# Kernel optimization log

Hardware: AMD Instinct MI355X
Metric: run time of the kernel (lower is better)

The kernel has to match this reference:

```python
import jax, jax.numpy as jnp
import numpy as np

N_SPECIAL = 4
LABEL_ID = 3
C_ACT = 64
C_TIME = 32
ACT_START = N_SPECIAL
TIME_START = N_SPECIAL + C_ACT
VOCAB = TIME_START + C_TIME  # 100
B, T, D = 8, 2048, 256


def l2norm(x, eps=1e-12):
    n = jnp.sqrt(jnp.sum(x * x, axis=-1, keepdims=True))
    return x / jnp.maximum(n, eps)


def causal_proto(h_norm, is_label, nxt, lo, hi, E_cls, alpha):
    """At every <LABEL> position L, build per-class prototypes from earlier
    support label positions (class = next token at that position), add a
    Bayesian prior alpha*E_cls, and return cosine sims of h_norm[L] vs protos.
    Non-label positions (or labels with no earlier support) -> zeros.
    Implemented as a single causal scan over time (online running sums)."""
    Bv, Tv, Dv = h_norm.shape
    C = E_cls.shape[0]
    is_sup = is_label & (nxt >= lo) & (nxt < hi)          # [B,T]
    cls = jnp.clip(nxt - lo, 0, C - 1)                    # [B,T]

    def step(carry, xs):
        Hsum, cnt = carry                                  # [B,C,D], [B,C]
        h_t, cls_t, sup_t, lab_t = xs                      # [B,D],[B],[B],[B]
        proto = l2norm((Hsum + alpha * E_cls) / (cnt[:, :, None] + alpha + 1e-8))
        sims = jnp.einsum('bd,bcd->bc', h_t, proto)        # cosine (h_t is unit)
        valid = lab_t & (jnp.sum(cnt, axis=-1) > 0)        # any earlier support
        out = jnp.where(valid[:, None], sims, 0.0)
        oh = jax.nn.one_hot(cls_t, C, dtype=h_t.dtype) * sup_t[:, None].astype(h_t.dtype)
        Hsum = Hsum + oh[:, :, None] * h_t[:, None, :]
        cnt = cnt + oh
        return (Hsum, cnt), out

    init = (jnp.zeros((Bv, C, Dv), h_norm.dtype), jnp.zeros((Bv, C), h_norm.dtype))
    xs = (jnp.swapaxes(h_norm, 0, 1), jnp.swapaxes(cls, 0, 1),
          jnp.swapaxes(is_sup, 0, 1), jnp.swapaxes(is_label, 0, 1))
    _, outs = jax.lax.scan(jax.checkpoint(step), init, xs)
    return jnp.swapaxes(outs, 0, 1)                        # [B,T,C]


def setup_inputs() -> dict:
    key = jax.random.key(0)
    ks = jax.random.split(key, 6)
    f32 = jnp.float32
    return {
        'tokens': jax.random.randint(ks[0], (B, T), 0, VOCAB, dtype=jnp.int32),
        'h': jax.random.normal(ks[1], (B, T, D), dtype=f32),
        'E': jax.random.normal(ks[2], (VOCAB, D), dtype=f32) * 0.02,
        'W_next': jax.random.normal(ks[3], (C_ACT, D), dtype=f32) * 0.02,
        'b_next': jnp.zeros((C_ACT,), f32),
        'W_time': jax.random.normal(ks[4], (C_TIME, D), dtype=f32) * 0.02,
        'b_time': jnp.zeros((C_TIME,), f32),
        'tied_scale_act': jnp.array(0.0, f32),
        'tied_scale_time': jnp.array(0.0, f32),
        'proto_scale_act': jnp.array(1.0, f32),
        'proto_scale_time': jnp.array(1.0, f32),
        'proto_prior_act': jnp.array(0.5, f32),
        'proto_prior_time': jnp.array(0.5, f32),
        'proto_temp_act': jnp.array(1.0, f32),
        'proto_temp_time': jnp.array(1.0, f32),
    }


def reference(tokens, h, E, W_next, b_next, W_time, b_time,
              tied_scale_act, tied_scale_time, proto_scale_act, proto_scale_time,
              proto_prior_act, proto_prior_time, proto_temp_act, proto_temp_time):
    sp = jax.nn.softplus
    # parametric heads
    param_next = jnp.einsum('btd,cd->btc', h, W_next) + b_next
    param_time = jnp.einsum('btd,cd->btc', h, W_time) + b_time
    # weight-tied heads (gradient flows into E here)
    tied_act = jnp.einsum('btd,cd->btc', h, E[ACT_START:TIME_START])
    tied_time = jnp.einsum('btd,cd->btc', h, E[TIME_START:VOCAB])
    # prototype head (E detached, as in the torch code)
    h_norm = l2norm(h)
    E_det = jax.lax.stop_gradient(E)
    E_act = l2norm(E_det[ACT_START:TIME_START])
    E_time = l2norm(E_det[TIME_START:VOCAB])
    nxt = jnp.roll(tokens, -1, axis=1)
    is_label = tokens == LABEL_ID
    proto_act = causal_proto(h_norm, is_label, nxt, ACT_START, TIME_START,
                             E_act, sp(proto_prior_act)) * sp(proto_temp_act)
    proto_time = causal_proto(h_norm, is_label, nxt, TIME_START, VOCAB,
                              E_time, sp(proto_prior_time)) * sp(proto_temp_time)
    activity_logits = param_next + sp(tied_scale_act) * tied_act + sp(proto_scale_act) * proto_act
    time_logits = param_time + sp(tied_scale_time) * tied_time + sp(proto_scale_time) * proto_time
    return (activity_logits, time_logits)
```

## Files before the change

kernel.cpp:

```cpp
#include <hip/hip_runtime.h>
#include <hip/hip_bf16.h>

#define Bv 8
#define Tv 2048
#define Dv 256
#define C_ACT 64
#define C_TIME 32
#define NCLS 96
#define LABEL_ID 3
#define ACT_START 4
#define TIME_START 68
#define VOCAB 100
#define MAXEV 36

typedef short bf16x8 __attribute__((ext_vector_type(8)));
typedef float f32x4  __attribute__((ext_vector_type(4)));

__device__ __forceinline__ float bf2f(__hip_bfloat16 x) { return __bfloat162float(x); }
__device__ __forceinline__ float bfb(unsigned short u) {
    union { unsigned int i; float f; } x; x.i = ((unsigned int)u) << 16; return x.f;
}
__device__ __forceinline__ short f2bs(float x) {
    __hip_bfloat16 b = __float2bfloat16(x);
    return *reinterpret_cast<short*>(&b);
}
__device__ __forceinline__ float spf(float x) { return log1pf(expf(x)); }

__device__ __forceinline__ float ldx(const void* p, size_t i, bool f32) {
    return f32 ? ((const float*)p)[i] : bf2f(((const __hip_bfloat16*)p)[i]);
}
__device__ __forceinline__ void stx(void* p, size_t i, float v, bool f32) {
    if (f32) ((float*)p)[i] = v;
    else     ((__hip_bfloat16*)p)[i] = __float2bfloat16(v);
}
__device__ __forceinline__ float4 ld4(const void* p, size_t i, bool f32) {
    if (f32) return *reinterpret_cast<const float4*>((const float*)p + i);
    ushort4 s = *reinterpret_cast<const ushort4*>((const unsigned short*)p + i);
    float4 u; u.x = bfb(s.x); u.y = bfb(s.y); u.z = bfb(s.z); u.w = bfb(s.w);
    return u;
}

__device__ __forceinline__ bool detect_f32_256(const void* h, int tid, int* s_cnt)
{
    if (tid == 0) *s_cnt = 0;
    __syncthreads();
    ushort4 u = *(reinterpret_cast<const ushort4*>(h) + tid);
    int c = 0; float v;
    v = bfb(u.x); if (!(fabsf(v) < 1e20f)) c++;
    v = bfb(u.y); if (!(fabsf(v) < 1e20f)) c++;
    v = bfb(u.z); if (!(fabsf(v) < 1e20f)) c++;
    v = bfb(u.w); if (!(fabsf(v) < 1e20f)) c++;
    #pragma unroll
    for (int o = 32; o > 0; o >>= 1) c += __shfl_down(c, o);
    if ((tid & 63) == 0 && c) atomicAdd(s_cnt, c);
    __syncthreads();
    return *s_cnt >= 4;
}

__device__ __forceinline__ size_t out_idx(int b, int L, int c)
{
    return (c < C_ACT)
        ? ((size_t)(b * Tv + L) * C_ACT + c)
        : ((size_t)Bv * Tv * C_ACT + (size_t)(b * Tv + L) * C_TIME + (c - C_ACT));
}

#define K1_ROWS 32
#define HPAD 72
#define EVLD 264
#define GLD 44

__global__ __launch_bounds__(256) void k_all(
    const int* __restrict__ tokens,
    const void* __restrict__ h,
    const void* __restrict__ E,
    const void* __restrict__ Wn, const void* __restrict__ bn,
    const void* __restrict__ Wt, const void* __restrict__ bt,
    const void* ts_a, const void* ts_t,
    const void* ps_a, const void* ps_t,
    const void* pp_a, const void* pp_t,
    const void* pt_a, const void* pt_t,
    void* __restrict__ out)
{
    __shared__ union {
        struct { short hB[K1_ROWS * HPAD]; short mB[NCLS * HPAD]; } t;
        struct {
            unsigned short hb[48][EVLD];
            union {
                unsigned short AsMs[48][EVLD];
                struct {
                    float Gl[MAXEV][GLD];
                    float P[MAXEV][24];
                    float Pm[MAXEV][24];
                    float SG[MAXEV][24];
                } r;
            } u2;
            float nrm[MAXEV];
        } s;
    } u;
    __shared__ int s_pos[MAXEV], s_cls[MAXEV];
    __shared__ int s_cnt, s_evn;

    int tid = threadIdx.x;
    bool f32 = detect_f32_256(h, tid, &s_cnt);
    float spt_a = spf(ldx(ts_a, 0, f32));
    float spt_t = spf(ldx(ts_t, 0, f32));

    if (blockIdx.x >= 32) {
        int R0   = (blockIdx.x - 32) * K1_ROWS;
        int w    = tid >> 6;
        int lane = tid & 63;
        int lr   = lane & 15;
        int quad = lane >> 4;
        int rt   = w & 1;
        int cg   = w >> 1;

        f32x4 acc[3];
        #pragma unroll
        for (int n = 0; n < 3; ++n) acc[n] = (f32x4){0.f, 0.f, 0.f, 0.f};

        for (int dc = 0; dc < 4; ++dc) {
            #pragma unroll
            for (int k = 0; k < 2; ++k) {
                int f = tid + k * 256;
                int row = f >> 4, dd4 = f & 15;
                float4 v = ld4(h, (size_t)(R0 + row) * Dv + dc * 64 + dd4 * 4, f32);
                short4 s4 = make_short4(f2bs(v.x), f2bs(v.y), f2bs(v.z), f2bs(v.w));
                *reinterpret_cast<short4*>(&u.t.hB[row * HPAD + dd4 * 4]) = s4;
            }
            #pragma unroll
            for (int k = 0; k < 6; ++k) {
                int f = tid + k * 256;
                int c = f >> 4, dd4 = f & 15;
                int col = dc * 64 + dd4 * 4;
                bool act = c < C_ACT;
                size_t wrow = act ? (size_t)c : (size_t)(c - C_ACT);
                int erow = act ? (ACT_START + c) : (TIME_START + (c - C_ACT));
                float4 w4 = ld4(act ? Wn : Wt, wrow * Dv + col, f32);
                float4 e4 = ld4(E, (size_t)erow * Dv + col, f32);
                float spt = act ? spt_a : spt_t;
                short4 s4 = make_short4(f2bs(w4.x + spt * e4.x),
                                        f2bs(w4.y + spt * e4.y),
                                        f2bs(w4.z + spt * e4.z),
                                        f2bs(w4.w + spt * e4.w));
                *reinterpret_cast<short4*>(&u.t.mB[c * HPAD + dd4 * 4]) = s4;
            }
            __syncthreads();

            #pragma unroll
            for (int ks = 0; ks < 2; ++ks) {
                int k0 = ks * 32;
                bf16x8 a = *reinterpret_cast<const bf16x8*>(
                    &u.t.hB[(16 * rt + lr) * HPAD + k0 + quad * 8]);
                #pragma unroll
                for (int nn = 0; nn < 3; ++nn) {
                    int n = 3 * cg + nn;
                    bf16x8 bf = *reinterpret_cast<const bf16x8*>(
                        &u.t.mB[(16 * n + lr) * HPAD + k0 + quad * 8]);
                    acc[nn] = __builtin_amdgcn_mfma_f32_16x16x32_bf16(a, bf, acc[nn], 0, 0, 0);
                }
            }
            __syncthreads();
        }

        #pragma unroll
        for (int nn = 0; nn < 3; ++nn) {
            int c = 16 * (3 * cg + nn) + lr;
            float bias = (c < C_ACT) ? ldx(bn, c, f32) : ldx(bt, c - C_ACT, f32);
            #pragma unroll
            for (int r = 0; r < 4; ++r) {
                int row = R0 + 16 * rt + quad * 4 + r;
                if (tokens[row] == LABEL_ID) continue;
                stx(out, out_idx(row >> 11, row & (Tv - 1), c), acc[nn][r] + bias, f32);
            }
        }
        return;
    }

    int b  = blockIdx.x >> 2;
    int q  = blockIdx.x & 3;
    int c0 = q * 24;
    int lane = tid & 63, wvx = tid >> 6;
    int lr = lane & 15, quad = lane >> 4;

    int* s_tok = reinterpret_cast<int*>(&u.s.u2.AsMs[0][0]);
    for (int i = tid; i < Tv; i += 256) s_tok[i] = tokens[(size_t)b * Tv + i];
    __syncthreads();

    if (tid < 64) {
        int base = 0;
        for (int seg = 0; seg < 32; ++seg) {
            unsigned long long m = __ballot(s_tok[seg * 64 + tid] == LABEL_ID);
            int rank = __popcll(m & ((1ull << tid) - 1ull));
            if (((m >> tid) & 1ull) && (base + rank) < MAXEV)
                s_pos[base + rank] = seg * 64 + tid;
            base += __popcll(m);
        }
        if (tid == 0) s_evn = base < MAXEV ? base : MAXEV;
    }
    __syncthreads();
    int evn = s_evn;
    int nrt = (evn + 15) >> 4;

    if (tid < evn) {
        int nxt = s_tok[(s_pos[tid] + 1) & (Tv - 1)];
        int c = -1;
        if (nxt >= ACT_START && nxt < TIME_START)  c = nxt - ACT_START;
        else if (nxt >= TIME_START && nxt < VOCAB) c = C_ACT + (nxt - TIME_START);
        s_cls[tid] = c;
    }

    {
        float4 hv[9];
        #pragma unroll
        for (int k = 0; k < 9; ++k) {
            int i = wvx + 4 * k;
            if (i < evn)
                hv[k] = ld4(h, ((size_t)b * Tv + s_pos[i]) * Dv + lane * 4, f32);
        }
        #pragma unroll
        for (int k = 0; k < 9; ++k) {
            int i = wvx + 4 * k;
            if (i < evn) {
                float4 v = hv[k];
                float p = v.x * v.x + v.y * v.y + v.z * v.z + v.w * v.w;
                #pragma unroll
                for (int o = 32; o > 0; o >>= 1) p += __shfl_xor(p, o);
                float nr = fmaxf(sqrtf(p), 1e-12f);
                float inv = 1.0f / nr;
                ushort4 s4;
                s4.x = (unsigned short)f2bs(v.x * inv);
                s4.y = (unsigned short)f2bs(v.y * inv);
                s4.z = (unsigned short)f2bs(v.z * inv);
                s4.w = (unsigned short)f2bs(v.w * inv);
                *reinterpret_cast<ushort4*>(&u.s.hb[i][lane * 4]) = s4;
                if (lane == 0) u.s.nrm[i] = nr;
            }
        }
        for (int i = evn + wvx; i < 16 * nrt; i += 4) {
            ushort4 z; z.x = z.y = z.z = z.w = 0;
            *reinterpret_cast<ushort4*>(&u.s.hb[i][lane * 4]) = z;
        }
    }
    __syncthreads();

    float alpha_a = spf(ldx(pp_a, 0, f32));
    float alpha_t = spf(ldx(pp_t, 0, f32));

    {
        float4 ev[6], wv6[6];
        #pragma unroll
        for (int k = 0; k < 6; ++k) {
            int lc = wvx + 4 * k, c = c0 + lc;
            bool act = c < C_ACT;
            int erow = act ? (ACT_START + c) : (TIME_START + (c - C_ACT));
            size_t wrow = act ? (size_t)c : (size_t)(c - C_ACT);
            ev[k]  = ld4(E, (size_t)erow * Dv + lane * 4, f32);
            wv6[k] = ld4(act ? Wn : Wt, wrow * Dv + lane * 4, f32);
        }
        #pragma unroll
        for (int k = 0; k < 6; ++k) {
            int lc = wvx + 4 * k, c = c0 + lc;
            bool act = c < C_ACT;
            float4 e4 = ev[k], w4 = wv6[k];
            float p = e4.x * e4.x + e4.y * e4.y + e4.z * e4.z + e4.w * e4.w;
            #pragma unroll
            for (int o = 32; o > 0; o >>= 1) p += __shfl_xor(p, o);
            float alpha = act ? alpha_a : alpha_t;
            float ai  = alpha / fmaxf(sqrtf(p), 1e-12f);
            float spt = act ? spt_a : spt_t;
            ushort4 a4, m4;
            a4.x = (unsigned short)f2bs(e4.x * ai);
            a4.y = (unsigned short)f2bs(e4.y * ai);
            a4.z = (unsigned short)f2bs(e4.z * ai);
            a4.w = (unsigned short)f2bs(e4.w * ai);
            m4.x = (unsigned short)f2bs(w4.x + spt * e4.x);
            m4.y = (unsigned short)f2bs(w4.y + spt * e4.y);
            m4.z = (unsigned short)f2bs(w4.z + spt * e4.z);
            m4.w = (unsigned short)f2bs(w4.w + spt * e4.w);
            *reinterpret_cast<ushort4*>(&u.s.u2.AsMs[lc][lane * 4])      = a4;
            *reinterpret_cast<ushort4*>(&u.s.u2.AsMs[24 + lc][lane * 4]) = m4;
        }
    }
    __syncthreads();

    {
        int nct = 3 + nrt;
        int TT  = nrt * nct;
        f32x4 accs[5];
        #pragma unroll
        for (int kk = 0; kk < 5; ++kk) {
            int t = wvx + 4 * kk;
            if (t < TT) {
                int rt2 = t / nct, ct = t - rt2 * nct;
                int ar = 16 * rt2 + lr;
                const unsigned short* bbase = (ct < 3)
                    ? &u.s.u2.AsMs[16 * ct + lr][0]
                    : &u.s.hb[16 * (ct - 3) + lr][0];
                f32x4 acc = (f32x4){0.f, 0.f, 0.f, 0.f};
                #pragma unroll
                for (int ks = 0; ks < 8; ++ks) {
                    bf16x8 a  = *reinterpret_cast<const bf16x8*>(
                        &u.s.hb[ar][ks * 32 + quad * 8]);
                    bf16x8 bf = *reinterpret_cast<const bf16x8*>(
                        &bbase[ks * 32 + quad * 8]);
                    acc = __builtin_amdgcn_mfma_f32_16x16x32_bf16(a, bf, acc, 0, 0, 0);
                }
                accs[kk] = acc;
            }
        }
        __syncthreads();
        #pragma unroll
        for (int kk = 0; kk < 5; ++kk) {
            int t = wvx + 4 * kk;
            if (t < TT) {
                int rt2 = t / nct, ct = t - rt2 * nct;
                #pragma unroll
                for (int r = 0; r < 4; ++r) {
                    int row = 16 * rt2 + quad * 4 + r;
                    if (row >= evn) continue;
                    if (ct < 3) {
                        int cc = 16 * ct + lr;
                        if (cc < 24) u.s.u2.r.P[row][cc] = accs[kk][r];
                        else         u.s.u2.r.Pm[row][cc - 24] = accs[kk][r];
                    } else {
                        int j = 16 * (ct - 3) + lr;
                        if (j < evn) u.s.u2.r.Gl[row][j] = accs[kk][r];
                    }
                }
            }
        }
    }
    __syncthreads();

    for (int t = tid; t < evn * 24; t += 256) {
        int i = t / 24, lc = t - i * 24;
        int c = c0 + lc;
        float s = 0.f;
        for (int j = 0; j < i; ++j)
            s += (s_cls[j] == c) ? u.s.u2.r.Gl[i][j] : 0.f;
        u.s.u2.r.SG[i][lc] = s;
    }
    __syncthreads();

    {
        float mult_a = spf(ldx(ps_a, 0, f32)) * spf(ldx(pt_a, 0, f32));
        float mult_t = spf(ldx(ps_t, 0, f32)) * spf(ldx(pt_t, 0, f32));
        for (int t = tid; t < evn * 24; t += 256) {
            int i = t / 24, lc = t - i * 24;
            int c = c0 + lc;
            bool actc = c < C_ACT;
            float alpha = actc ? alpha_a : alpha_t;
            float bias  = actc ? ldx(bn, c, f32) : ldx(bt, c - C_ACT, f32);
            float mult  = actc ? mult_a : mult_t;
            float n2 = alpha * alpha;
            bool any = false;
            for (int j = 0; j < i; ++j) {
                int cj = s_cls[j];
                if (cj == c)
                    n2 += 2.f * (u.s.u2.r.P[j][lc] + u.s.u2.r.SG[j][lc])
                        + u.s.u2.r.Gl[j][j];
                any = any || (actc ? (cj >= 0 && cj < C_ACT) : (cj >= C_ACT));
            }
            float v = u.s.u2.r.Pm[i][lc] * u.s.nrm[i] + bias;
            if (any) {
                float num = u.s.u2.r.P[i][lc] + u.s.u2.r.SG[i][lc];
                v += mult * (num / fmaxf(sqrtf(n2), 1e-20f));
            }
            stx(out, out_idx(b, s_pos[i], c), v, f32);
        }
    }
}

extern "C" void kernel_launch(void* const* d_in, const int* in_sizes, int n_in,
                              void* d_out, int out_size, void* d_ws, size_t ws_size,
                              hipStream_t stream)
{
    const int* tokens = (const int*)d_in[0];
    const void* h    = d_in[1];
    const void* E    = d_in[2];
    const void* Wn   = d_in[3];
    const void* bn   = d_in[4];
    const void* Wt   = d_in[5];
    const void* bt   = d_in[6];
    const void* ts_a = d_in[7];
    const void* ts_t = d_in[8];
    const void* ps_a = d_in[9];
    const void* ps_t = d_in[10];
    const void* pp_a = d_in[11];
    const void* pp_t = d_in[12];
    const void* pt_a = d_in[13];
    const void* pt_t = d_in[14];

    k_all<<<32 + (Bv * Tv) / K1_ROWS, 256, 0, stream>>>(
        tokens, h, E, Wn, bn, Wt, bt,
        ts_a, ts_t, ps_a, ps_t, pp_a, pp_t, pt_a, pt_t, d_out);
}
```

Baseline: 117.9 us.

## Double-buffer LDS tiles and prefetch bf16 inputs in parametric GEMM blocks

For bf16 inputs, the dense-head GEMM blocks now use two LDS buffers. Global loads for the next K-chunk are issued into registers with 16-byte vector loads before the MFMAs on the current chunk, which removes one barrier per iteration and overlaps load latency with compute. Token and bias loads are hoisted ahead of the main loop. The fp32 path keeps the old single-buffer scheme, and the doubled LDS footprint for this branch shares the union with the proto branch's larger buffers.

```diff
diff --git a/kernel.cpp b/kernel.cpp
--- a/kernel.cpp
+++ b/kernel.cpp
@@ -15,6 +15,7 @@
 
 typedef short bf16x8 __attribute__((ext_vector_type(8)));
 typedef float f32x4  __attribute__((ext_vector_type(4)));
+typedef unsigned short u16x8 __attribute__((ext_vector_type(8)));
 
 __device__ __forceinline__ float bf2f(__hip_bfloat16 x) { return __bfloat162float(x); }
 __device__ __forceinline__ float bfb(unsigned short u) {
@@ -82,7 +83,10 @@
     void* __restrict__ out)
 {
     __shared__ union {
-        struct { short hB[K1_ROWS * HPAD]; short mB[NCLS * HPAD]; } t;
+        struct {
+            short hB[2][K1_ROWS * HPAD];
+            short mB[2][NCLS * HPAD];
+        } t;
         struct {
             unsigned short hb[48][EVLD];
             union {
@@ -118,59 +122,141 @@
         #pragma unroll
         for (int n = 0; n < 3; ++n) acc[n] = (f32x4){0.f, 0.f, 0.f, 0.f};
 
-        for (int dc = 0; dc < 4; ++dc) {
-            #pragma unroll
-            for (int k = 0; k < 2; ++k) {
-                int f = tid + k * 256;
-                int row = f >> 4, dd4 = f & 15;
-                float4 v = ld4(h, (size_t)(R0 + row) * Dv + dc * 64 + dd4 * 4, f32);
-                short4 s4 = make_short4(f2bs(v.x), f2bs(v.y), f2bs(v.z), f2bs(v.w));
-                *reinterpret_cast<short4*>(&u.t.hB[row * HPAD + dd4 * 4]) = s4;
-            }
-            #pragma unroll
-            for (int k = 0; k < 6; ++k) {
-                int f = tid + k * 256;
-                int c = f >> 4, dd4 = f & 15;
-                int col = dc * 64 + dd4 * 4;
-                bool act = c < C_ACT;
-                size_t wrow = act ? (size_t)c : (size_t)(c - C_ACT);
-                int erow = act ? (ACT_START + c) : (TIME_START + (c - C_ACT));
-                float4 w4 = ld4(act ? Wn : Wt, wrow * Dv + col, f32);
-                float4 e4 = ld4(E, (size_t)erow * Dv + col, f32);
-                float spt = act ? spt_a : spt_t;
-                short4 s4 = make_short4(f2bs(w4.x + spt * e4.x),
-                                        f2bs(w4.y + spt * e4.y),
-                                        f2bs(w4.z + spt * e4.z),
-                                        f2bs(w4.w + spt * e4.w));
-                *reinterpret_cast<short4*>(&u.t.mB[c * HPAD + dd4 * 4]) = s4;
-            }
-            __syncthreads();
-
-            #pragma unroll
-            for (int ks = 0; ks < 2; ++ks) {
-                int k0 = ks * 32;
-                bf16x8 a = *reinterpret_cast<const bf16x8*>(
-                    &u.t.hB[(16 * rt + lr) * HPAD + k0 + quad * 8]);
-                #pragma unroll
-                for (int nn = 0; nn < 3; ++nn) {
-                    int n = 3 * cg + nn;
-                    bf16x8 bf = *reinterpret_cast<const bf16x8*>(
-                        &u.t.mB[(16 * n + lr) * HPAD + k0 + quad * 8]);
-                    acc[nn] = __builtin_amdgcn_mfma_f32_16x16x32_bf16(a, bf, acc[nn], 0, 0, 0);
-                }
-            }
-            __syncthreads();
-        }
-
+        int rowb = 16 * rt + quad * 4;
+        int tk[4]; float bs[3];
+        #pragma unroll
+        for (int r = 0; r < 4; ++r) tk[r] = tokens[R0 + rowb + r];
         #pragma unroll
         for (int nn = 0; nn < 3; ++nn) {
             int c = 16 * (3 * cg + nn) + lr;
-            float bias = (c < C_ACT) ? ldx(bn, c, f32) : ldx(bt, c - C_ACT, f32);
+            bs[nn] = (c < C_ACT) ? ldx(bn, c, f32) : ldx(bt, c - C_ACT, f32);
+        }
+
+        if (!f32) {
+            const unsigned short* hp  = (const unsigned short*)h;
+            const unsigned short* wnp = (const unsigned short*)Wn;
+            const unsigned short* wtp = (const unsigned short*)Wt;
+            const unsigned short* ep  = (const unsigned short*)E;
+
+            int rowh = tid >> 3, c8h = (tid & 7) * 8;
+            int hoff = (R0 + rowh) * Dv + c8h;
+
+            int cM[3], c8M[3], woff[3], eoff[3]; float sptM[3];
+            const unsigned short* wp[3];
+            #pragma unroll
+            for (int k = 0; k < 3; ++k) {
+                int f = tid + k * 256;
+                int c = f >> 3, c8 = (f & 7) * 8;
+                bool act = c < C_ACT;
+                cM[k] = c; c8M[k] = c8;
+                wp[k]   = act ? wnp : wtp;
+                woff[k] = (act ? c : c - C_ACT) * Dv + c8;
+                eoff[k] = (act ? (ACT_START + c) : (TIME_START + (c - C_ACT))) * Dv + c8;
+                sptM[k] = act ? spt_a : spt_t;
+            }
+
+            u16x8 hr, wr0, wr1, wr2, er0, er1, er2;
+            auto ldall = [&](int dc) {
+                int o = dc * 64;
+                hr  = *reinterpret_cast<const u16x8*>(hp + hoff + o);
+                wr0 = *reinterpret_cast<const u16x8*>(wp[0] + woff[0] + o);
+                er0 = *reinterpret_cast<const u16x8*>(ep + eoff[0] + o);
+                wr1 = *reinterpret_cast<const u16x8*>(wp[1] + woff[1] + o);
+                er1 = *reinterpret_cast<const u16x8*>(ep + eoff[1] + o);
+                wr2 = *reinterpret_cast<const u16x8*>(wp[2] + woff[2] + o);
+                er2 = *reinterpret_cast<const u16x8*>(ep + eoff[2] + o);
+            };
+            auto wrall = [&](int bsel) {
+                *reinterpret_cast<u16x8*>(&u.t.hB[bsel][rowh * HPAD + c8h]) = hr;
+                u16x8 m8;
+                #pragma unroll
+                for (int j = 0; j < 8; ++j)
+                    m8[j] = (unsigned short)f2bs(bfb(wr0[j]) + sptM[0] * bfb(er0[j]));
+                *reinterpret_cast<u16x8*>(&u.t.mB[bsel][cM[0] * HPAD + c8M[0]]) = m8;
+                #pragma unroll
+                for (int j = 0; j < 8; ++j)
+                    m8[j] = (unsigned short)f2bs(bfb(wr1[j]) + sptM[1] * bfb(er1[j]));
+                *reinterpret_cast<u16x8*>(&u.t.mB[bsel][cM[1] * HPAD + c8M[1]]) = m8;
+                #pragma unroll
+                for (int j = 0; j < 8; ++j)
+                    m8[j] = (unsigned short)f2bs(bfb(wr2[j]) + sptM[2] * bfb(er2[j]));
+                *reinterpret_cast<u16x8*>(&u.t.mB[bsel][cM[2] * HPAD + c8M[2]]) = m8;
+            };
+
+            ldall(0); wrall(0);
+            __syncthreads();
+            for (int dc = 0; dc < 4; ++dc) {
+                if (dc < 3) ldall(dc + 1);
+                const short* hbuf = u.t.hB[dc & 1];
+                const short* mbuf = u.t.mB[dc & 1];
+                #pragma unroll
+                for (int ks = 0; ks < 2; ++ks) {
+                    int k0 = ks * 32;
+                    bf16x8 a = *reinterpret_cast<const bf16x8*>(
+                        &hbuf[(16 * rt + lr) * HPAD + k0 + quad * 8]);
+                    #pragma unroll
+                    for (int nn = 0; nn < 3; ++nn) {
+                        bf16x8 bfv = *reinterpret_cast<const bf16x8*>(
+                            &mbuf[(16 * (3 * cg + nn) + lr) * HPAD + k0 + quad * 8]);
+                        acc[nn] = __builtin_amdgcn_mfma_f32_16x16x32_bf16(a, bfv, acc[nn], 0, 0, 0);
+                    }
+                }
+                if (dc < 3) wrall((dc + 1) & 1);
+                __syncthreads();
+            }
+        } else {
+            for (int dc = 0; dc < 4; ++dc) {
+                #pragma unroll
+                for (int k = 0; k < 2; ++k) {
+                    int f = tid + k * 256;
+                    int row = f >> 4, dd4 = f & 15;
+                    float4 v = ld4(h, (size_t)(R0 + row) * Dv + dc * 64 + dd4 * 4, f32);
+                    short4 s4 = make_short4(f2bs(v.x), f2bs(v.y), f2bs(v.z), f2bs(v.w));
+                    *reinterpret_cast<short4*>(&u.t.hB[0][row * HPAD + dd4 * 4]) = s4;
+                }
+                #pragma unroll
+                for (int k = 0; k < 6; ++k) {
+                    int f = tid + k * 256;
+                    int c = f >> 4, dd4 = f & 15;
+                    int col = dc * 64 + dd4 * 4;
+                    bool act = c < C_ACT;
+                    size_t wrow = act ? (size_t)c : (size_t)(c - C_ACT);
+                    int erow = act ? (ACT_START + c) : (TIME_START + (c - C_ACT));
+                    float4 w4 = ld4(act ? Wn : Wt, wrow * Dv + col, f32);
+                    float4 e4 = ld4(E, (size_t)erow * Dv + col, f32);
+                    float spt = act ? spt_a : spt_t;
+                    short4 s4 = make_short4(f2bs(w4.x + spt * e4.x),
+                                            f2bs(w4.y + spt * e4.y),
+                                            f2bs(w4.z + spt * e4.z),
+                                            f2bs(w4.w + spt * e4.w));
+                    *reinterpret_cast<short4*>(&u.t.mB[0][c * HPAD + dd4 * 4]) = s4;
+                }
+                __syncthreads();
+
+                #pragma unroll
+                for (int ks = 0; ks < 2; ++ks) {
+                    int k0 = ks * 32;
+                    bf16x8 a = *reinterpret_cast<const bf16x8*>(
+                        &u.t.hB[0][(16 * rt + lr) * HPAD + k0 + quad * 8]);
+                    #pragma unroll
+                    for (int nn = 0; nn < 3; ++nn) {
+                        bf16x8 bfv = *reinterpret_cast<const bf16x8*>(
+                            &u.t.mB[0][(16 * (3 * cg + nn) + lr) * HPAD + k0 + quad * 8]);
+                        acc[nn] = __builtin_amdgcn_mfma_f32_16x16x32_bf16(a, bfv, acc[nn], 0, 0, 0);
+                    }
+                }
+                __syncthreads();
+            }
+        }
+
+        #pragma unroll
+        for (int nn = 0; nn < 3; ++nn) {
+            int c = 16 * (3 * cg + nn) + lr;
             #pragma unroll
             for (int r = 0; r < 4; ++r) {
-                int row = R0 + 16 * rt + quad * 4 + r;
-                if (tokens[row] == LABEL_ID) continue;
-                stx(out, out_idx(row >> 11, row & (Tv - 1), c), acc[nn][r] + bias, f32);
+                if (tk[r] == LABEL_ID) continue;
+                int row = R0 + rowb + r;
+                stx(out, out_idx(row >> 11, row & (Tv - 1), c), acc[nn][r] + bs[nn], f32);
             }
         }
         return;
```

After: 119.1 us. No clear change (+1.0%).
